# Kernel tuning notes

Hardware: AMD Instinct MI355X
Metric: run time of the kernel (lower is better)

## Reference

```python
import jax, jax.numpy as jnp
import numpy as np

N, D = 262144, 512
EPS = 1e-6  # flax LayerNorm default


def setup_inputs() -> dict:
    key = jax.random.key(0)
    kx, kw = jax.random.split(key)
    x = jax.random.normal(kx, (N, D), dtype=jnp.float32)
    # LayerNorm params (flax defaults: scale init ones, bias init zeros)
    ln_scale = jnp.ones((D,), dtype=jnp.float32)
    ln_bias = jnp.zeros((D,), dtype=jnp.float32)
    # Dense params (lecun_normal kernel init approximated by scaled normal)
    kernel = jax.random.normal(kw, (D, D), dtype=jnp.float32) / jnp.sqrt(jnp.float32(D))
    bias = jnp.zeros((D,), dtype=jnp.float32)
    return {"x": x, "ln_scale": ln_scale, "ln_bias": ln_bias, "kernel": kernel, "bias": bias}


def reference(x, ln_scale, ln_bias, kernel, bias):
    # LayerNorm over last axis
    mu = jnp.mean(x, axis=-1, keepdims=True)
    var = jnp.mean(jnp.square(x - mu), axis=-1, keepdims=True)
    out = (x - mu) * jax.lax.rsqrt(var + EPS) * ln_scale + ln_bias
    # activation -> Dense -> residual add
    h = jax.nn.relu(out)
    return x + jnp.dot(h, kernel) + bias
```

## Files before the change

### kernel.cpp

```cpp
#include <hip/hip_runtime.h>
#include <hip/hip_bf16.h>

#define DD 512
#define BM 32
#define THREADS 512

typedef __attribute__((ext_vector_type(8))) short short8;
typedef __attribute__((ext_vector_type(4))) float f32x4;

__device__ __forceinline__ unsigned short f2bf(float f) {
  union { float f; unsigned u; } v; v.f = f;
  unsigned r = v.u + 0x7FFFu + ((v.u >> 16) & 1u);
  return (unsigned short)(r >> 16);
}

__global__ void prep_bpack(const float* __restrict__ W, unsigned short* __restrict__ Bpack) {
  const int tid = blockIdx.x * blockDim.x + threadIdx.x;
  const int n = tid & 511, k = tid >> 9;
  const float w = W[(size_t)k * DD + n];
  const int nb = n >> 4, lo = n & 15;
  const int kt = k >> 5, hi = (k >> 3) & 3, j = k & 7;
  const int lane = hi * 16 + lo;
  Bpack[(((size_t)(nb * 16 + kt)) * 64 + lane) * 8 + j] = f2bf(w);
}

__global__ __launch_bounds__(THREADS, 6)
void fused_ln_gemm(const float* __restrict__ x, const float* __restrict__ lns,
                   const float* __restrict__ lnb, const unsigned short* __restrict__ Bpack,
                   const float* __restrict__ bias, float* __restrict__ out) {
  __shared__ unsigned short Alds[BM * 512];

  const int t = threadIdx.x;
  const long row0 = (long)blockIdx.x * BM;

  {
    const int r = t >> 4, g = t & 15;
    const float* xr = x + (row0 + r) * DD + g * 4;
    float4 v[8];
    float s = 0.f, s2 = 0.f;
    #pragma unroll
    for (int i = 0; i < 8; ++i) {
      v[i] = *(const float4*)(xr + i * 64);
      s  += (v[i].x + v[i].y) + (v[i].z + v[i].w);
      s2 += v[i].x * v[i].x + v[i].y * v[i].y + v[i].z * v[i].z + v[i].w * v[i].w;
    }
    #pragma unroll
    for (int m = 1; m < 16; m <<= 1) {
      s  += __shfl_xor(s,  m, 64);
      s2 += __shfl_xor(s2, m, 64);
    }
    const float mu   = s * (1.f / 512.f);
    const float var  = fmaxf(s2 * (1.f / 512.f) - mu * mu, 0.f);
    const float rstd = rsqrtf(var + 1e-6f);
    #pragma unroll
    for (int i = 0; i < 8; ++i) {
      const int c = g * 4 + i * 64;
      const float4 sc = *(const float4*)(lns + c);
      const float4 bi = *(const float4*)(lnb + c);
      ushort4 hu;
      hu.x = f2bf(fmaxf((v[i].x - mu) * rstd * sc.x + bi.x, 0.f));
      hu.y = f2bf(fmaxf((v[i].y - mu) * rstd * sc.y + bi.y, 0.f));
      hu.z = f2bf(fmaxf((v[i].z - mu) * rstd * sc.z + bi.z, 0.f));
      hu.w = f2bf(fmaxf((v[i].w - mu) * rstd * sc.w + bi.w, 0.f));
      const unsigned a = (unsigned)(r * 1024 + g * 8 + i * 128) ^ (unsigned)((r & 7) << 4);
      *(ushort4*)((char*)Alds + a) = hu;
    }
  }
  __syncthreads();

  const int lane = t & 63, lo = lane & 15, hi = lane >> 4;
  const int wn = t >> 6;

  const float* xc = x + (row0 + hi * 4) * DD + wn * 64 + lo;
  const float bv0 = bias[wn * 64 +  0 + lo];
  const float bv1 = bias[wn * 64 + 16 + lo];
  const float bv2 = bias[wn * 64 + 32 + lo];
  const float bv3 = bias[wn * 64 + 48 + lo];

  f32x4 acc00, acc01, acc02, acc03, acc10, acc11, acc12, acc13;
  #pragma unroll
  for (int q = 0; q < 4; ++q) {
    const float* r0 = xc + q * DD;
    const float* r1 = xc + (16 * DD) + q * DD;
    acc00[q] = r0[ 0] + bv0;  acc01[q] = r0[16] + bv1;
    acc02[q] = r0[32] + bv2;  acc03[q] = r0[48] + bv3;
    acc10[q] = r1[ 0] + bv0;  acc11[q] = r1[16] + bv1;
    acc12[q] = r1[32] + bv2;  acc13[q] = r1[48] + bv3;
  }

  unsigned abase0, aswz0, abase1, aswz1;
  {
    const int r0 = lo;       abase0 = (unsigned)(r0 * 1024 + hi * 16); aswz0 = (unsigned)((r0 & 7) << 4);
    const int r1 = 16 + lo;  abase1 = (unsigned)(r1 * 1024 + hi * 16); aswz1 = (unsigned)((r1 & 7) << 4);
  }
  const short8* bbase = (const short8*)Bpack + (size_t)wn * 4096 + lane;

  #pragma unroll
  for (int kt = 0; kt < 16; ++kt) {
    const short8 b0 = bbase[(0 * 16 + kt) * 64];
    const short8 b1 = bbase[(1 * 16 + kt) * 64];
    const short8 b2 = bbase[(2 * 16 + kt) * 64];
    const short8 b3 = bbase[(3 * 16 + kt) * 64];
    const short8 a0 = *(const short8*)((const char*)Alds + ((abase0 + (unsigned)kt * 64) ^ aswz0));
    const short8 a1 = *(const short8*)((const char*)Alds + ((abase1 + (unsigned)kt * 64) ^ aswz1));
    acc00 = __builtin_amdgcn_mfma_f32_16x16x32_bf16(a0, b0, acc00, 0, 0, 0);
    acc10 = __builtin_amdgcn_mfma_f32_16x16x32_bf16(a1, b0, acc10, 0, 0, 0);
    acc01 = __builtin_amdgcn_mfma_f32_16x16x32_bf16(a0, b1, acc01, 0, 0, 0);
    acc11 = __builtin_amdgcn_mfma_f32_16x16x32_bf16(a1, b1, acc11, 0, 0, 0);
    acc02 = __builtin_amdgcn_mfma_f32_16x16x32_bf16(a0, b2, acc02, 0, 0, 0);
    acc12 = __builtin_amdgcn_mfma_f32_16x16x32_bf16(a1, b2, acc12, 0, 0, 0);
    acc03 = __builtin_amdgcn_mfma_f32_16x16x32_bf16(a0, b3, acc03, 0, 0, 0);
    acc13 = __builtin_amdgcn_mfma_f32_16x16x32_bf16(a1, b3, acc13, 0, 0, 0);
  }

  float* oc = out + (row0 + hi * 4) * DD + wn * 64 + lo;
  #pragma unroll
  for (int q = 0; q < 4; ++q) {
    float* r0 = oc + q * DD;
    float* r1 = oc + (16 * DD) + q * DD;
    r0[ 0] = acc00[q];  r0[16] = acc01[q];  r0[32] = acc02[q];  r0[48] = acc03[q];
    r1[ 0] = acc10[q];  r1[16] = acc11[q];  r1[32] = acc12[q];  r1[48] = acc13[q];
  }
}

extern "C" void kernel_launch(void* const* d_in, const int* in_sizes, int n_in,
                              void* d_out, int out_size, void* d_ws, size_t ws_size,
                              hipStream_t stream) {
  const float* x    = (const float*)d_in[0];
  const float* lns  = (const float*)d_in[1];
  const float* lnb  = (const float*)d_in[2];
  const float* W    = (const float*)d_in[3];
  const float* bias = (const float*)d_in[4];
  float* out = (float*)d_out;
  unsigned short* Bpack = (unsigned short*)d_ws;

  const int nrows = in_sizes[0] / DD;

  prep_bpack<<<DD * DD / 256, 256, 0, stream>>>(W, Bpack);
  fused_ln_gemm<<<nrows / BM, THREADS, 0, stream>>>(x, lns, lnb, Bpack, bias, out);
}
```

Measured before the change: 362.9 us.

## Double row tile to 64 per block and preload residual before barrier

New measurement: 411.9 us. +13.5%, slower.

```diff
diff --git a/kernel.cpp b/kernel.cpp
--- a/kernel.cpp
+++ b/kernel.cpp
@@ -2,7 +2,7 @@
 #include <hip/hip_bf16.h>
 
 #define DD 512
-#define BM 32
+#define BM 64
 #define THREADS 512
 
 typedef __attribute__((ext_vector_type(8))) short short8;
@@ -24,17 +24,20 @@
   Bpack[(((size_t)(nb * 16 + kt)) * 64 + lane) * 8 + j] = f2bf(w);
 }
 
-__global__ __launch_bounds__(THREADS, 6)
+__global__ __launch_bounds__(THREADS, 4)
 void fused_ln_gemm(const float* __restrict__ x, const float* __restrict__ lns,
                    const float* __restrict__ lnb, const unsigned short* __restrict__ Bpack,
                    const float* __restrict__ bias, float* __restrict__ out) {
   __shared__ unsigned short Alds[BM * 512];
 
   const int t = threadIdx.x;
+  const int lane = t & 63, lo = lane & 15, hi = lane >> 4;
+  const int wn = t >> 6;
   const long row0 = (long)blockIdx.x * BM;
 
-  {
-    const int r = t >> 4, g = t & 15;
+  #pragma unroll
+  for (int m2 = 0; m2 < 2; ++m2) {
+    const int r = m2 * 32 + (t >> 4), g = t & 15;
     const float* xr = x + (row0 + r) * DD + g * 4;
     float4 v[8];
     float s = 0.f, s2 = 0.f;
@@ -66,60 +69,68 @@
       *(ushort4*)((char*)Alds + a) = hu;
     }
   }
-  __syncthreads();
 
-  const int lane = t & 63, lo = lane & 15, hi = lane >> 4;
-  const int wn = t >> 6;
-
-  const float* xc = x + (row0 + hi * 4) * DD + wn * 64 + lo;
   const float bv0 = bias[wn * 64 +  0 + lo];
   const float bv1 = bias[wn * 64 + 16 + lo];
   const float bv2 = bias[wn * 64 + 32 + lo];
   const float bv3 = bias[wn * 64 + 48 + lo];
 
-  f32x4 acc00, acc01, acc02, acc03, acc10, acc11, acc12, acc13;
+  f32x4 acc[4][4];
+  {
+    const float* xc = x + (row0 + hi * 4) * DD + wn * 64 + lo;
+    #pragma unroll
+    for (int m = 0; m < 4; ++m) {
+      #pragma unroll
+      for (int q = 0; q < 4; ++q) {
+        const float* r = xc + (m * 16 + q) * DD;
+        acc[m][0][q] = r[ 0] + bv0;
+        acc[m][1][q] = r[16] + bv1;
+        acc[m][2][q] = r[32] + bv2;
+        acc[m][3][q] = r[48] + bv3;
+      }
+    }
+  }
+  __syncthreads();
+
+  unsigned abase[4], aswz[4];
   #pragma unroll
-  for (int q = 0; q < 4; ++q) {
-    const float* r0 = xc + q * DD;
-    const float* r1 = xc + (16 * DD) + q * DD;
-    acc00[q] = r0[ 0] + bv0;  acc01[q] = r0[16] + bv1;
-    acc02[q] = r0[32] + bv2;  acc03[q] = r0[48] + bv3;
-    acc10[q] = r1[ 0] + bv0;  acc11[q] = r1[16] + bv1;
-    acc12[q] = r1[32] + bv2;  acc13[q] = r1[48] + bv3;
-  }
-
-  unsigned abase0, aswz0, abase1, aswz1;
-  {
-    const int r0 = lo;       abase0 = (unsigned)(r0 * 1024 + hi * 16); aswz0 = (unsigned)((r0 & 7) << 4);
-    const int r1 = 16 + lo;  abase1 = (unsigned)(r1 * 1024 + hi * 16); aswz1 = (unsigned)((r1 & 7) << 4);
+  for (int m = 0; m < 4; ++m) {
+    const int r = m * 16 + lo;
+    abase[m] = (unsigned)(r * 1024 + hi * 16);
+    aswz[m]  = (unsigned)((r & 7) << 4);
   }
   const short8* bbase = (const short8*)Bpack + (size_t)wn * 4096 + lane;
 
   #pragma unroll
   for (int kt = 0; kt < 16; ++kt) {
-    const short8 b0 = bbase[(0 * 16 + kt) * 64];
-    const short8 b1 = bbase[(1 * 16 + kt) * 64];
-    const short8 b2 = bbase[(2 * 16 + kt) * 64];
-    const short8 b3 = bbase[(3 * 16 + kt) * 64];
-    const short8 a0 = *(const short8*)((const char*)Alds + ((abase0 + (unsigned)kt * 64) ^ aswz0));
-    const short8 a1 = *(const short8*)((const char*)Alds + ((abase1 + (unsigned)kt * 64) ^ aswz1));
-    acc00 = __builtin_amdgcn_mfma_f32_16x16x32_bf16(a0, b0, acc00, 0, 0, 0);
-    acc10 = __builtin_amdgcn_mfma_f32_16x16x32_bf16(a1, b0, acc10, 0, 0, 0);
-    acc01 = __builtin_amdgcn_mfma_f32_16x16x32_bf16(a0, b1, acc01, 0, 0, 0);
-    acc11 = __builtin_amdgcn_mfma_f32_16x16x32_bf16(a1, b1, acc11, 0, 0, 0);
-    acc02 = __builtin_amdgcn_mfma_f32_16x16x32_bf16(a0, b2, acc02, 0, 0, 0);
-    acc12 = __builtin_amdgcn_mfma_f32_16x16x32_bf16(a1, b2, acc12, 0, 0, 0);
-    acc03 = __builtin_amdgcn_mfma_f32_16x16x32_bf16(a0, b3, acc03, 0, 0, 0);
-    acc13 = __builtin_amdgcn_mfma_f32_16x16x32_bf16(a1, b3, acc13, 0, 0, 0);
+    const short8 b0 = bbase[0 * 1024 + kt * 64];
+    const short8 b1 = bbase[1 * 1024 + kt * 64];
+    const short8 b2 = bbase[2 * 1024 + kt * 64];
+    const short8 b3 = bbase[3 * 1024 + kt * 64];
+    short8 a[4];
+    #pragma unroll
+    for (int m = 0; m < 4; ++m)
+      a[m] = *(const short8*)((const char*)Alds + ((abase[m] + (unsigned)kt * 64) ^ aswz[m]));
+    #pragma unroll
+    for (int m = 0; m < 4; ++m) {
+      acc[m][0] = __builtin_amdgcn_mfma_f32_16x16x32_bf16(a[m], b0, acc[m][0], 0, 0, 0);
+      acc[m][1] = __builtin_amdgcn_mfma_f32_16x16x32_bf16(a[m], b1, acc[m][1], 0, 0, 0);
+      acc[m][2] = __builtin_amdgcn_mfma_f32_16x16x32_bf16(a[m], b2, acc[m][2], 0, 0, 0);
+      acc[m][3] = __builtin_amdgcn_mfma_f32_16x16x32_bf16(a[m], b3, acc[m][3], 0, 0, 0);
+    }
   }
 
   float* oc = out + (row0 + hi * 4) * DD + wn * 64 + lo;
   #pragma unroll
-  for (int q = 0; q < 4; ++q) {
-    float* r0 = oc + q * DD;
-    float* r1 = oc + (16 * DD) + q * DD;
-    r0[ 0] = acc00[q];  r0[16] = acc01[q];  r0[32] = acc02[q];  r0[48] = acc03[q];
-    r1[ 0] = acc10[q];  r1[16] = acc11[q];  r1[32] = acc12[q];  r1[48] = acc13[q];
+  for (int m = 0; m < 4; ++m) {
+    #pragma unroll
+    for (int q = 0; q < 4; ++q) {
+      float* r = oc + (m * 16 + q) * DD;
+      r[ 0] = acc[m][0][q];
+      r[16] = acc[m][1][q];
+      r[32] = acc[m][2][q];
+      r[48] = acc[m][3][q];
+    }
   }
 }
 
```

## Double block threads so each wave computes a 32x32 output tile

Applied to the files above, without the earlier changes.

After: 391.8 us. +8.0%, slower.

```diff
diff --git a/kernel.cpp b/kernel.cpp
--- a/kernel.cpp
+++ b/kernel.cpp
@@ -3,7 +3,7 @@
 
 #define DD 512
 #define BM 32
-#define THREADS 512
+#define THREADS 1024
 
 typedef __attribute__((ext_vector_type(8))) short short8;
 typedef __attribute__((ext_vector_type(4))) float f32x4;
@@ -24,28 +24,30 @@
   Bpack[(((size_t)(nb * 16 + kt)) * 64 + lane) * 8 + j] = f2bf(w);
 }
 
-__global__ __launch_bounds__(THREADS, 6)
+__global__ __launch_bounds__(THREADS, 8)
 void fused_ln_gemm(const float* __restrict__ x, const float* __restrict__ lns,
                    const float* __restrict__ lnb, const unsigned short* __restrict__ Bpack,
                    const float* __restrict__ bias, float* __restrict__ out) {
   __shared__ unsigned short Alds[BM * 512];
 
   const int t = threadIdx.x;
+  const int lane = t & 63, lo = lane & 15, hi = lane >> 4;
+  const int w = t >> 6;
   const long row0 = (long)blockIdx.x * BM;
 
   {
-    const int r = t >> 4, g = t & 15;
+    const int r = t >> 5, g = t & 31;
     const float* xr = x + (row0 + r) * DD + g * 4;
-    float4 v[8];
+    float4 v[4];
     float s = 0.f, s2 = 0.f;
     #pragma unroll
-    for (int i = 0; i < 8; ++i) {
-      v[i] = *(const float4*)(xr + i * 64);
+    for (int i = 0; i < 4; ++i) {
+      v[i] = *(const float4*)(xr + i * 128);
       s  += (v[i].x + v[i].y) + (v[i].z + v[i].w);
       s2 += v[i].x * v[i].x + v[i].y * v[i].y + v[i].z * v[i].z + v[i].w * v[i].w;
     }
     #pragma unroll
-    for (int m = 1; m < 16; m <<= 1) {
+    for (int m = 1; m < 32; m <<= 1) {
       s  += __shfl_xor(s,  m, 64);
       s2 += __shfl_xor(s2, m, 64);
     }
@@ -53,8 +55,8 @@
     const float var  = fmaxf(s2 * (1.f / 512.f) - mu * mu, 0.f);
     const float rstd = rsqrtf(var + 1e-6f);
     #pragma unroll
-    for (int i = 0; i < 8; ++i) {
-      const int c = g * 4 + i * 64;
+    for (int i = 0; i < 4; ++i) {
+      const int c = g * 4 + i * 128;
       const float4 sc = *(const float4*)(lns + c);
       const float4 bi = *(const float4*)(lnb + c);
       ushort4 hu;
@@ -62,64 +64,56 @@
       hu.y = f2bf(fmaxf((v[i].y - mu) * rstd * sc.y + bi.y, 0.f));
       hu.z = f2bf(fmaxf((v[i].z - mu) * rstd * sc.z + bi.z, 0.f));
       hu.w = f2bf(fmaxf((v[i].w - mu) * rstd * sc.w + bi.w, 0.f));
-      const unsigned a = (unsigned)(r * 1024 + g * 8 + i * 128) ^ (unsigned)((r & 7) << 4);
+      const unsigned a = (unsigned)(r * 1024 + g * 8 + i * 256) ^ (unsigned)((r & 7) << 4);
       *(ushort4*)((char*)Alds + a) = hu;
+    }
+  }
+
+  const int col0 = w * 32 + lo;
+  const float bv0 = bias[col0];
+  const float bv1 = bias[col0 + 16];
+
+  f32x4 acc00, acc01, acc10, acc11;
+  {
+    const float* xc = x + (row0 + hi * 4) * DD + col0;
+    #pragma unroll
+    for (int q = 0; q < 4; ++q) {
+      const float* r0 = xc + q * DD;
+      const float* r1 = xc + 16 * DD + q * DD;
+      acc00[q] = r0[0]  + bv0;
+      acc01[q] = r0[16] + bv1;
+      acc10[q] = r1[0]  + bv0;
+      acc11[q] = r1[16] + bv1;
     }
   }
   __syncthreads();
 
-  const int lane = t & 63, lo = lane & 15, hi = lane >> 4;
-  const int wn = t >> 6;
-
-  const float* xc = x + (row0 + hi * 4) * DD + wn * 64 + lo;
-  const float bv0 = bias[wn * 64 +  0 + lo];
-  const float bv1 = bias[wn * 64 + 16 + lo];
-  const float bv2 = bias[wn * 64 + 32 + lo];
-  const float bv3 = bias[wn * 64 + 48 + lo];
-
-  f32x4 acc00, acc01, acc02, acc03, acc10, acc11, acc12, acc13;
-  #pragma unroll
-  for (int q = 0; q < 4; ++q) {
-    const float* r0 = xc + q * DD;
-    const float* r1 = xc + (16 * DD) + q * DD;
-    acc00[q] = r0[ 0] + bv0;  acc01[q] = r0[16] + bv1;
-    acc02[q] = r0[32] + bv2;  acc03[q] = r0[48] + bv3;
-    acc10[q] = r1[ 0] + bv0;  acc11[q] = r1[16] + bv1;
-    acc12[q] = r1[32] + bv2;  acc13[q] = r1[48] + bv3;
-  }
-
-  unsigned abase0, aswz0, abase1, aswz1;
-  {
-    const int r0 = lo;       abase0 = (unsigned)(r0 * 1024 + hi * 16); aswz0 = (unsigned)((r0 & 7) << 4);
-    const int r1 = 16 + lo;  abase1 = (unsigned)(r1 * 1024 + hi * 16); aswz1 = (unsigned)((r1 & 7) << 4);
-  }
-  const short8* bbase = (const short8*)Bpack + (size_t)wn * 4096 + lane;
+  const unsigned ab0 = (unsigned)(lo * 1024 + hi * 16);
+  const unsigned ab1 = (unsigned)((16 + lo) * 1024 + hi * 16);
+  const unsigned asw = (unsigned)((lo & 7) << 4);
+  const short8* bb = (const short8*)Bpack + (size_t)(w * 2) * 1024 + lane;
 
   #pragma unroll
   for (int kt = 0; kt < 16; ++kt) {
-    const short8 b0 = bbase[(0 * 16 + kt) * 64];
-    const short8 b1 = bbase[(1 * 16 + kt) * 64];
-    const short8 b2 = bbase[(2 * 16 + kt) * 64];
-    const short8 b3 = bbase[(3 * 16 + kt) * 64];
-    const short8 a0 = *(const short8*)((const char*)Alds + ((abase0 + (unsigned)kt * 64) ^ aswz0));
-    const short8 a1 = *(const short8*)((const char*)Alds + ((abase1 + (unsigned)kt * 64) ^ aswz1));
+    const short8 b0 = bb[kt * 64];
+    const short8 b1 = bb[1024 + kt * 64];
+    const short8 a0 = *(const short8*)((const char*)Alds + ((ab0 + (unsigned)kt * 64) ^ asw));
+    const short8 a1 = *(const short8*)((const char*)Alds + ((ab1 + (unsigned)kt * 64) ^ asw));
     acc00 = __builtin_amdgcn_mfma_f32_16x16x32_bf16(a0, b0, acc00, 0, 0, 0);
+    acc01 = __builtin_amdgcn_mfma_f32_16x16x32_bf16(a0, b1, acc01, 0, 0, 0);
     acc10 = __builtin_amdgcn_mfma_f32_16x16x32_bf16(a1, b0, acc10, 0, 0, 0);
-    acc01 = __builtin_amdgcn_mfma_f32_16x16x32_bf16(a0, b1, acc01, 0, 0, 0);
     acc11 = __builtin_amdgcn_mfma_f32_16x16x32_bf16(a1, b1, acc11, 0, 0, 0);
-    acc02 = __builtin_amdgcn_mfma_f32_16x16x32_bf16(a0, b2, acc02, 0, 0, 0);
-    acc12 = __builtin_amdgcn_mfma_f32_16x16x32_bf16(a1, b2, acc12, 0, 0, 0);
-    acc03 = __builtin_amdgcn_mfma_f32_16x16x32_bf16(a0, b3, acc03, 0, 0, 0);
-    acc13 = __builtin_amdgcn_mfma_f32_16x16x32_bf16(a1, b3, acc13, 0, 0, 0);
   }
 
-  float* oc = out + (row0 + hi * 4) * DD + wn * 64 + lo;
+  float* oc = out + (row0 + hi * 4) * DD + col0;
   #pragma unroll
   for (int q = 0; q < 4; ++q) {
     float* r0 = oc + q * DD;
-    float* r1 = oc + (16 * DD) + q * DD;
-    r0[ 0] = acc00[q];  r0[16] = acc01[q];  r0[32] = acc02[q];  r0[48] = acc03[q];
-    r1[ 0] = acc10[q];  r1[16] = acc11[q];  r1[32] = acc12[q];  r1[48] = acc13[q];
+    float* r1 = oc + 16 * DD + q * DD;
+    r0[0]  = acc00[q];
+    r0[16] = acc01[q];
+    r1[0]  = acc10[q];
+    r1[16] = acc11[q];
   }
 }
 
```
